# Optimization experiments

Measured on AMD Instinct MI355X. Metric: run time of the kernel, lower is better.

The kernel has to match this reference:

```python
import jax, jax.numpy as jnp
import numpy as np

B, S, D_IN, D_OUT = 4, 2048, 2048, 2048
E, R, TOP_K = 8, 8, 2
ALPHA = 16.0
SCALE = ALPHA / R  # alpha / r


def setup_inputs() -> dict:
    key = jax.random.key(0)
    ks = jax.random.split(key, 6)
    x = jax.random.normal(ks[0], (B, S, D_IN), dtype=jnp.float32)
    # base frozen linear: torch Linear weight [out, in], bias [out]
    W_base = jax.random.normal(ks[1], (D_OUT, D_IN), dtype=jnp.float32) / np.sqrt(D_IN)
    b_base = jax.random.normal(ks[2], (D_OUT,), dtype=jnp.float32) * 0.01
    # router: Linear(in_features, num_experts, bias=False) -> weight [E, in]
    W_router = jax.random.normal(ks[3], (E, D_IN), dtype=jnp.float32) / np.sqrt(D_IN)
    # LoRA experts: A [E, r, in], B [E, out, r] (torch inits B to zero; use small
    # random values so outputs/grads are non-trivial -- math is identical)
    A_w = jax.random.normal(ks[4], (E, R, D_IN), dtype=jnp.float32) / np.sqrt(D_IN)
    B_w = jax.random.normal(ks[5], (E, D_OUT, R), dtype=jnp.float32) * 0.02
    return {"x": x, "W_base": W_base, "b_base": b_base,
            "W_router": W_router, "A_w": A_w, "B_w": B_w}


def reference(x, W_base, b_base, W_router, A_w, B_w):
    # frozen base linear: [B,S,out]
    y = jnp.einsum('bsd,od->bso', x, W_base) + b_base
    # router: logits [B,S,E] -> top-k + softmax over the k selected logits
    logits = jnp.einsum('bsd,ed->bse', x, W_router)
    topk_vals, topk_idx = jax.lax.top_k(logits, TOP_K)       # [B,S,k]
    gates = jax.nn.softmax(topk_vals, axis=-1)               # [B,S,k]
    # all-experts LoRA compute (matches the original dense-stack semantics)
    h = jnp.einsum('bsd,erd->bser', x, A_w)                  # [B,S,E,r]
    expert_outs = jnp.einsum('bser,eor->bseo', h, B_w) * SCALE  # [B,S,E,out]
    # gather the top-k expert outputs and combine with gates
    topk_outs = jnp.take_along_axis(expert_outs, topk_idx[..., None], axis=2)  # [B,S,k,out]
    fused = jnp.sum(topk_outs * gates[..., None], axis=2)    # [B,S,out]
    return y + fused
```

## Files before the change

### kernel.cpp

```cpp
#include <hip/hip_runtime.h>

typedef unsigned short u16;
typedef __attribute__((ext_vector_type(8))) short short8;
typedef __attribute__((ext_vector_type(4))) float f32x4;

#define GLL16(g, l) __builtin_amdgcn_global_load_lds(                         \
    (const __attribute__((address_space(1))) void*)(g),                        \
    (__attribute__((address_space(3))) void*)(l), 16, 0, 0)

__device__ __forceinline__ u16 f2bf(float f) {
  union { float f; unsigned u; } v; v.f = f;
  unsigned u = v.u;
  return (u16)((u + 0x7FFFu + ((u >> 16) & 1u)) >> 16);
}

__device__ __forceinline__ float bf2f(u16 u) {
  union { unsigned u; float f; } v; v.u = ((unsigned)u) << 16;
  return v.f;
}

__device__ __forceinline__ ushort4 cvt4(float4 v) {
  ushort4 o; o.x = f2bf(v.x); o.y = f2bf(v.y); o.z = f2bf(v.z); o.w = f2bf(v.w);
  return o;
}

__global__ __launch_bounds__(512) void k_pre(
    const float* __restrict__ x, const float* __restrict__ Wr,
    const float* __restrict__ Wb, const float* __restrict__ Aw,
    const float* __restrict__ Bw,
    u16* __restrict__ xbf, float* __restrict__ logits,
    u16* __restrict__ wbf, u16* __restrict__ aabf, u16* __restrict__ bmt)
{
  __shared__ float wlds[16384];
  {
    const float4* src = (const float4*)Wr;
    float4* dst = (float4*)wlds;
    int t = threadIdx.x;
#pragma unroll
    for (int i = 0; i < 8; ++i) dst[t + i * 512] = src[t + i * 512];
  }
  __syncthreads();
  const int wave = threadIdx.x >> 6, lane = threadIdx.x & 63;
  const float4* wv = (const float4*)wlds;
#pragma unroll 1
  for (int s = 0; s < 2; ++s) {
    int tok = blockIdx.x * 16 + wave * 2 + s;
    const float4* xrow = (const float4*)(x + tok * 2048);
    ushort4* orow = (ushort4*)(xbf + tok * 2048);
    float acc[8];
#pragma unroll
    for (int e = 0; e < 8; ++e) acc[e] = 0.f;
#pragma unroll 1
    for (int i = 0; i < 8; ++i) {
      float4 xv = xrow[lane + i * 64];
      orow[lane + i * 64] = cvt4(xv);
#pragma unroll
      for (int e = 0; e < 8; ++e) {
        float4 b = wv[e * 512 + lane + i * 64];
        acc[e] += xv.x * b.x + xv.y * b.y + xv.z * b.z + xv.w * b.w;
      }
    }
#pragma unroll
    for (int e = 0; e < 8; ++e) {
      float v = acc[e];
#pragma unroll
      for (int off = 32; off > 0; off >>= 1) v += __shfl_xor(v, off, 64);
      acc[e] = v;
    }
    if (lane == 0) {
#pragma unroll
      for (int e = 0; e < 8; ++e) logits[tok * 8 + e] = acc[e];
    }
  }
  const int tidg = blockIdx.x * 512 + threadIdx.x;
  {
    const float4* src = (const float4*)Wb;
    ushort4* dst = (ushort4*)wbf;
#pragma unroll
    for (int i = 0; i < 4; ++i)
      dst[tidg + i * 262144] = cvt4(src[tidg + i * 262144]);
  }
  if (tidg < 32768) {
    ((ushort4*)aabf)[tidg] = cvt4(((const float4*)Aw)[tidg]);
  }
  if (tidg < 2048) {
    const int n = tidg;
#pragma unroll
    for (int e = 0; e < 8; ++e) {
      const float4* src = (const float4*)(Bw + e * 16384 + n * 8);
      ushort4* dst = (ushort4*)(bmt + n * 64 + e * 8);
      dst[0] = cvt4(src[0]);
      dst[1] = cvt4(src[1]);
    }
  }
}

__global__ __launch_bounds__(256) void k_hgemm(
    const u16* __restrict__ xbf, const u16* __restrict__ aabf,
    u16* __restrict__ P)
{
  __shared__ u16 As[256 * 64];
  __shared__ u16 Bs[64 * 64];
  int t = threadIdx.x, wave = t >> 6, lane = t & 63;
  int mBase = blockIdx.x * 256;
  int ks = blockIdx.y;
  int fr = lane & 15, fg = lane >> 4;
  int lrow = lane >> 3, lcol = (lane & 7) * 8;
  f32x4 zero = {0.f, 0.f, 0.f, 0.f};
  f32x4 acc[4][4];
#pragma unroll
  for (int i = 0; i < 4; ++i)
#pragma unroll
    for (int j = 0; j < 4; ++j) acc[i][j] = zero;
#pragma unroll 1
  for (int it = 0; it < 4; ++it) {
    int k0 = ks * 256 + it * 64;
    __syncthreads();
#pragma unroll
    for (int cc = 0; cc < 8; ++cc) {
      int c = wave * 8 + cc;
      GLL16(xbf + (mBase + c * 8 + lrow) * 2048 + k0 + lcol, &As[c * 512]);
    }
#pragma unroll
    for (int cc = 0; cc < 2; ++cc) {
      int c = wave * 2 + cc;
      GLL16(aabf + (c * 8 + lrow) * 2048 + k0 + lcol, &Bs[c * 512]);
    }
    __syncthreads();
#pragma unroll
    for (int kk = 0; kk < 2; ++kk) {
      short8 a[4], bfr[4];
#pragma unroll
      for (int i = 0; i < 4; ++i)
        a[i] = *(const short8*)&As[(wave * 64 + i * 16 + fr) * 64 + kk * 32 + fg * 8];
#pragma unroll
      for (int j = 0; j < 4; ++j)
        bfr[j] = *(const short8*)&Bs[(j * 16 + fr) * 64 + kk * 32 + fg * 8];
#pragma unroll
      for (int i = 0; i < 4; ++i)
#pragma unroll
        for (int j = 0; j < 4; ++j)
          acc[i][j] = __builtin_amdgcn_mfma_f32_16x16x32_bf16(a[i], bfr[j], acc[i][j], 0, 0, 0);
    }
  }
#pragma unroll
  for (int i = 0; i < 4; ++i)
#pragma unroll
    for (int j = 0; j < 4; ++j)
#pragma unroll
      for (int r = 0; r < 4; ++r) {
        int m = mBase + wave * 64 + i * 16 + fg * 4 + r;
        int n = j * 16 + fr;
        P[(ks * 8192 + m) * 64 + n] = f2bf(acc[i][j][r]);
      }
}

__global__ __launch_bounds__(256) void k_topk(
    const float* __restrict__ logits, const u16* __restrict__ P,
    u16* __restrict__ G)
{
  int t = threadIdx.x, wave = t >> 6, lane = t & 63;
  int tok = blockIdx.x * 4 + wave;
  const float* lg = logits + tok * 8;
  float la[8];
#pragma unroll
  for (int e = 0; e < 8; ++e) la[e] = lg[e];
  float v0 = la[0]; int i0 = 0;
#pragma unroll
  for (int e = 1; e < 8; ++e) { if (la[e] > v0) { v0 = la[e]; i0 = e; } }
  float v1 = -3.4e38f; int i1 = 0;
#pragma unroll
  for (int e = 0; e < 8; ++e) { if (e != i0 && la[e] > v1) { v1 = la[e]; i1 = e; } }
  float ex = expf(v1 - v0);
  float inv = 1.f / (1.f + ex);
  float gate0 = inv, gate1 = ex * inv;
  int e = lane >> 3;
  float h = 0.f;
#pragma unroll
  for (int ks = 0; ks < 8; ++ks) h += bf2f(P[(ks * 8192 + tok) * 64 + lane]);
  float g = (e == i0) ? gate0 : ((e == i1) ? gate1 : 0.f);
  G[tok * 64 + lane] = f2bf(2.0f * g * h);
}

__global__ __launch_bounds__(256, 2) void k_main(
    const u16* __restrict__ xbf, const u16* __restrict__ wbf,
    const u16* __restrict__ G, const u16* __restrict__ BmT,
    const float* __restrict__ bias, float* __restrict__ out)
{
  __shared__ u16 lds[40960];
  const int tid = threadIdx.x;
  const int w = tid >> 6, lane = tid & 63;
  const int fr = lane & 15, fg = lane >> 4;
  const int wr = w >> 1, wc = w & 1;

  const int b0 = blockIdx.x;
  const int xcd = b0 & 7, i = b0 >> 3;
  const int mBase = (xcd * 8 + (i >> 3)) * 128;
  const int nBase = (i & 7) * 256;

  const int rl = lane >> 3;
  const int ce = ((lane & 7) ^ rl) << 3;
  const int swz = (fr & 7) << 3;
  const int colk0 = (fg * 8) ^ swz;
  const int colk1 = (32 + fg * 8) ^ swz;
  const int aOff = (wr * 64 + fr) * 64;
  const int bOff = (wc * 128 + fr) * 64;

  const u16* pA = xbf + (mBase + w * 8 + rl) * 2048 + ce;
  const u16* pB = wbf + (nBase + w * 8 + rl) * 2048 + ce;

  f32x4 acc[4][8];
  const f32x4 zero = {0.f, 0.f, 0.f, 0.f};
#pragma unroll
  for (int mi = 0; mi < 4; ++mi)
#pragma unroll
    for (int nj = 0; nj < 8; ++nj) acc[mi][nj] = zero;

  short8 a[4][2];
  short8 U[2][2], V[2][2];

#define LGKM(N) asm volatile("s_waitcnt lgkmcnt(" #N ")" ::: "memory")
#define VMC(N)  asm volatile("s_waitcnt vmcnt(" #N ")" ::: "memory")
#define BAR()   __builtin_amdgcn_s_barrier()

#define SA() { GLL16(pA,          lds + w * 512);                             \
               GLL16(pA + 65536,  lds + 2048 + w * 512);                      \
               GLL16(pA + 131072, lds + 4096 + w * 512);                      \
               GLL16(pA + 196608, lds + 6144 + w * 512);                      \
               pA += 64; }
#define SB_LO(BOFF) { GLL16(pB,          lds + (BOFF) + w * 512);             \
                      GLL16(pB + 65536,  lds + (BOFF) + 2048 + w * 512);      \
                      GLL16(pB + 131072, lds + (BOFF) + 4096 + w * 512);      \
                      GLL16(pB + 196608, lds + (BOFF) + 6144 + w * 512); }
#define SB_HI(BOFF) { GLL16(pB + 262144, lds + (BOFF) + 8192 + w * 512);      \
                      GLL16(pB + 327680, lds + (BOFF) + 10240 + w * 512);     \
                      GLL16(pB + 393216, lds + (BOFF) + 12288 + w * 512);     \
                      GLL16(pB + 458752, lds + (BOFF) + 14336 + w * 512);     \
                      pB += 64; }

#define RDA()                                                                 \
  _Pragma("unroll")                                                           \
  for (int mi = 0; mi < 4; ++mi) {                                            \
    a[mi][0] = *(const short8*)(lds + aOff + mi * 1024 + colk0);              \
    a[mi][1] = *(const short8*)(lds + aOff + mi * 1024 + colk1);              \
  }

#define RDB2(DST, BOFF, NJ0)                                                  \
  DST[0][0] = *(const short8*)(lds + (BOFF) + bOff + (NJ0) * 1024 + colk0);   \
  DST[0][1] = *(const short8*)(lds + (BOFF) + bOff + (NJ0) * 1024 + colk1);   \
  DST[1][0] = *(const short8*)(lds + (BOFF) + bOff + ((NJ0)+1) * 1024 + colk0);\
  DST[1][1] = *(const short8*)(lds + (BOFF) + bOff + ((NJ0)+1) * 1024 + colk1);

#define MFMAP(BV, NJ0)                                                        \
  __builtin_amdgcn_s_setprio(1);                                              \
  _Pragma("unroll")                                                           \
  for (int kk = 0; kk < 2; ++kk)                                              \
    _Pragma("unroll")                                                         \
    for (int mi = 0; mi < 4; ++mi)                                            \
      _Pragma("unroll")                                                       \
      for (int j = 0; j < 2; ++j)                                             \
        acc[mi][(NJ0) + j] = __builtin_amdgcn_mfma_f32_16x16x32_bf16(         \
            a[mi][kk], BV[j][kk], acc[mi][(NJ0) + j], 0, 0, 0);               \
  __builtin_amdgcn_s_setprio(0);

#define TILE(BCUR, BNXT, SA_STMT, SBL_STMT, SBH_STMT)                         \
  {                                                                           \
                                                                      \
    VMC(0);                                                                   \
    BAR();                                                                    \
    RDB2(U, BCUR, 0)                                                          \
    RDA()                                                                     \
    RDB2(V, BCUR, 2)                                                          \
    LGKM(4);                                                                  \
    MFMAP(U, 0)                                                               \
    BAR();                                                                    \
                                                                      \
    SA_STMT                                                                   \
    RDB2(U, BCUR, 4)                                                          \
    LGKM(4);                                                                  \
    MFMAP(V, 2)                                                               \
                                                                      \
    SBL_STMT                                                                  \
    RDB2(V, BCUR, 6)                                                          \
    LGKM(4);                                                                  \
    MFMAP(U, 4)                                                               \
                                                                      \
    SBH_STMT                                                                  \
    LGKM(0);                                                                  \
    MFMAP(V, 6)                                                               \
  }

  SA()
  SB_LO(8192) SB_HI(8192)

#pragma unroll 1
  for (int tt = 0; tt < 15; ++tt) {
    TILE(8192, 24576, SA(), SB_LO(24576), SB_HI(24576))
    TILE(24576, 8192, SA(), SB_LO(8192), SB_HI(8192))
  }
  TILE(8192, 24576, SA(), SB_LO(24576), SB_HI(24576))
  {
    const u16* pG = G + (mBase + w * 8 + rl) * 64 + ce;
    const u16* pT = BmT + (nBase + w * 8 + rl) * 64 + ce;
    TILE(24576, 8192,
         { GLL16(pG,        lds + w * 512);
           GLL16(pG + 2048, lds + 2048 + w * 512);
           GLL16(pG + 4096, lds + 4096 + w * 512);
           GLL16(pG + 6144, lds + 6144 + w * 512); },
         { GLL16(pT,        lds + 8192 + w * 512);
           GLL16(pT + 2048, lds + 8192 + 2048 + w * 512);
           GLL16(pT + 4096, lds + 8192 + 4096 + w * 512);
           GLL16(pT + 6144, lds + 8192 + 6144 + w * 512); },
         { GLL16(pT + 8192,  lds + 8192 + 8192 + w * 512);
           GLL16(pT + 10240, lds + 8192 + 10240 + w * 512);
           GLL16(pT + 12288, lds + 8192 + 12288 + w * 512);
           GLL16(pT + 14336, lds + 8192 + 14336 + w * 512); })
  }
  TILE(8192, 24576, {}, {}, {})

#pragma unroll
  for (int nj = 0; nj < 8; ++nj) {
    const int n = nBase + wc * 128 + nj * 16 + fr;
    const float bv = bias[n];
#pragma unroll
    for (int mi = 0; mi < 4; ++mi) {
      const int m = mBase + wr * 64 + mi * 16 + fg * 4;
#pragma unroll
      for (int r = 0; r < 4; ++r)
        out[(m + r) * 2048 + n] = acc[mi][nj][r] + bv;
    }
  }
#undef TILE
#undef MFMAP
#undef RDB2
#undef RDA
#undef SB_HI
#undef SB_LO
#undef SA
#undef BAR
#undef VMC
#undef LGKM
}

extern "C" void kernel_launch(void* const* d_in, const int* in_sizes, int n_in,
                              void* d_out, int out_size, void* d_ws, size_t ws_size,
                              hipStream_t stream) {
  const float* x  = (const float*)d_in[0];
  const float* Wb = (const float*)d_in[1];
  const float* bb = (const float*)d_in[2];
  const float* Wr = (const float*)d_in[3];
  const float* Aw = (const float*)d_in[4];
  const float* Bw = (const float*)d_in[5];

  char* ws = (char*)d_ws;
  u16*   xbf  = (u16*)  (ws + 0);
  u16*   wbf  = (u16*)  (ws + 33554432);
  u16*   aabf = (u16*)  (ws + 41943040);
  u16*   bmt  = (u16*)  (ws + 42205184);
  float* lgt  = (float*)(ws + 42467328);
  u16*   G    = (u16*)  (ws + 42729472);
  u16*   P   = (u16*)d_out;
  float* out = (float*)d_out;

  hipLaunchKernelGGL(k_pre,   dim3(512),   dim3(512), 0, stream,
                     x, Wr, Wb, Aw, Bw, xbf, lgt, wbf, aabf, bmt);
  hipLaunchKernelGGL(k_hgemm, dim3(32, 8), dim3(256), 0, stream, xbf, aabf, P);
  hipLaunchKernelGGL(k_topk,  dim3(2048),  dim3(256), 0, stream, lgt, P, G);
  hipLaunchKernelGGL(k_main,  dim3(512),   dim3(256), 0, stream,
                     xbf, wbf, G, bmt, bb, out);
}
```

Measured before the change: 108.9 us.

## Shrink main GEMM tile to 128x128 and raise occupancy to three blocks

```diff
diff --git a/kernel.cpp b/kernel.cpp
--- a/kernel.cpp
+++ b/kernel.cpp
@@ -182,21 +182,21 @@
   G[tok * 64 + lane] = f2bf(2.0f * g * h);
 }
 
-__global__ __launch_bounds__(256, 2) void k_main(
+__global__ __launch_bounds__(256, 3) void k_main(
     const u16* __restrict__ xbf, const u16* __restrict__ wbf,
     const u16* __restrict__ G, const u16* __restrict__ BmT,
     const float* __restrict__ bias, float* __restrict__ out)
 {
-  __shared__ u16 lds[40960];
+  __shared__ u16 lds[24576];
   const int tid = threadIdx.x;
   const int w = tid >> 6, lane = tid & 63;
   const int fr = lane & 15, fg = lane >> 4;
   const int wr = w >> 1, wc = w & 1;
 
   const int b0 = blockIdx.x;
-  const int xcd = b0 & 7, i = b0 >> 3;
-  const int mBase = (xcd * 8 + (i >> 3)) * 128;
-  const int nBase = (i & 7) * 256;
+  const int xcd = b0 & 7, ii = b0 >> 3;
+  const int mBase = (xcd * 8 + (ii >> 4)) * 128;
+  const int nBase = (ii & 15) * 128;
 
   const int rl = lane >> 3;
   const int ce = ((lane & 7) ^ rl) << 3;
@@ -204,17 +204,17 @@
   const int colk0 = (fg * 8) ^ swz;
   const int colk1 = (32 + fg * 8) ^ swz;
   const int aOff = (wr * 64 + fr) * 64;
-  const int bOff = (wc * 128 + fr) * 64;
-
-  const u16* pA = xbf + (mBase + w * 8 + rl) * 2048 + ce;
-  const u16* pB = wbf + (nBase + w * 8 + rl) * 2048 + ce;
-
-  f32x4 acc[4][8];
+  const int bOff = (wc * 64 + fr) * 64;
+
+  const u16* pA = xbf + (mBase + w * 32 + rl) * 2048 + ce;
+  const u16* pB = wbf + (nBase + w * 32 + rl) * 2048 + ce;
+
+  f32x4 acc[4][4];
   const f32x4 zero = {0.f, 0.f, 0.f, 0.f};
 #pragma unroll
   for (int mi = 0; mi < 4; ++mi)
 #pragma unroll
-    for (int nj = 0; nj < 8; ++nj) acc[mi][nj] = zero;
+    for (int nj = 0; nj < 4; ++nj) acc[mi][nj] = zero;
 
   short8 a[4][2];
   short8 U[2][2], V[2][2];
@@ -223,20 +223,16 @@
 #define VMC(N)  asm volatile("s_waitcnt vmcnt(" #N ")" ::: "memory")
 #define BAR()   __builtin_amdgcn_s_barrier()
 
-#define SA() { GLL16(pA,          lds + w * 512);                             \
-               GLL16(pA + 65536,  lds + 2048 + w * 512);                      \
-               GLL16(pA + 131072, lds + 4096 + w * 512);                      \
-               GLL16(pA + 196608, lds + 6144 + w * 512);                      \
+#define SA() { GLL16(pA,         lds + w * 2048);                             \
+               GLL16(pA + 16384, lds + w * 2048 + 512);                       \
+               GLL16(pA + 32768, lds + w * 2048 + 1024);                      \
+               GLL16(pA + 49152, lds + w * 2048 + 1536);                      \
                pA += 64; }
-#define SB_LO(BOFF) { GLL16(pB,          lds + (BOFF) + w * 512);             \
-                      GLL16(pB + 65536,  lds + (BOFF) + 2048 + w * 512);      \
-                      GLL16(pB + 131072, lds + (BOFF) + 4096 + w * 512);      \
-                      GLL16(pB + 196608, lds + (BOFF) + 6144 + w * 512); }
-#define SB_HI(BOFF) { GLL16(pB + 262144, lds + (BOFF) + 8192 + w * 512);      \
-                      GLL16(pB + 327680, lds + (BOFF) + 10240 + w * 512);     \
-                      GLL16(pB + 393216, lds + (BOFF) + 12288 + w * 512);     \
-                      GLL16(pB + 458752, lds + (BOFF) + 14336 + w * 512);     \
-                      pB += 64; }
+#define SB(BOFF) { GLL16(pB,         lds + (BOFF) + w * 2048);                \
+                   GLL16(pB + 16384, lds + (BOFF) + w * 2048 + 512);          \
+                   GLL16(pB + 32768, lds + (BOFF) + w * 2048 + 1024);         \
+                   GLL16(pB + 49152, lds + (BOFF) + w * 2048 + 1536);         \
+                   pB += 64; }
 
 #define RDA()                                                                 \
   _Pragma("unroll")                                                           \
@@ -263,7 +259,7 @@
             a[mi][kk], BV[j][kk], acc[mi][(NJ0) + j], 0, 0, 0);               \
   __builtin_amdgcn_s_setprio(0);
 
-#define TILE(BCUR, BNXT, SA_STMT, SBL_STMT, SBH_STMT)                         \
+#define TILE(BCUR, SBS, SAS)                                                  \
   {                                                                           \
                                                                       \
     VMC(0);                                                                   \
@@ -275,52 +271,39 @@
     MFMAP(U, 0)                                                               \
     BAR();                                                                    \
                                                                       \
-    SA_STMT                                                                   \
-    RDB2(U, BCUR, 4)                                                          \
-    LGKM(4);                                                                  \
+    SAS                                                                       \
+    SBS                                                                       \
+    LGKM(0);                                                                  \
     MFMAP(V, 2)                                                               \
-                                                                      \
-    SBL_STMT                                                                  \
-    RDB2(V, BCUR, 6)                                                          \
-    LGKM(4);                                                                  \
-    MFMAP(U, 4)                                                               \
-                                                                      \
-    SBH_STMT                                                                  \
-    LGKM(0);                                                                  \
-    MFMAP(V, 6)                                                               \
   }
 
   SA()
-  SB_LO(8192) SB_HI(8192)
+  SB(8192)
 
 #pragma unroll 1
   for (int tt = 0; tt < 15; ++tt) {
-    TILE(8192, 24576, SA(), SB_LO(24576), SB_HI(24576))
-    TILE(24576, 8192, SA(), SB_LO(8192), SB_HI(8192))
-  }
-  TILE(8192, 24576, SA(), SB_LO(24576), SB_HI(24576))
+    TILE(8192, SB(16384), SA())
+    TILE(16384, SB(8192), SA())
+  }
+  TILE(8192, SB(16384), SA())
   {
-    const u16* pG = G + (mBase + w * 8 + rl) * 64 + ce;
-    const u16* pT = BmT + (nBase + w * 8 + rl) * 64 + ce;
-    TILE(24576, 8192,
-         { GLL16(pG,        lds + w * 512);
-           GLL16(pG + 2048, lds + 2048 + w * 512);
-           GLL16(pG + 4096, lds + 4096 + w * 512);
-           GLL16(pG + 6144, lds + 6144 + w * 512); },
-         { GLL16(pT,        lds + 8192 + w * 512);
-           GLL16(pT + 2048, lds + 8192 + 2048 + w * 512);
-           GLL16(pT + 4096, lds + 8192 + 4096 + w * 512);
-           GLL16(pT + 6144, lds + 8192 + 6144 + w * 512); },
-         { GLL16(pT + 8192,  lds + 8192 + 8192 + w * 512);
-           GLL16(pT + 10240, lds + 8192 + 10240 + w * 512);
-           GLL16(pT + 12288, lds + 8192 + 12288 + w * 512);
-           GLL16(pT + 14336, lds + 8192 + 14336 + w * 512); })
-  }
-  TILE(8192, 24576, {}, {}, {})
-
-#pragma unroll
-  for (int nj = 0; nj < 8; ++nj) {
-    const int n = nBase + wc * 128 + nj * 16 + fr;
+    const u16* pG = G + (mBase + w * 32 + rl) * 64 + ce;
+    const u16* pT = BmT + (nBase + w * 32 + rl) * 64 + ce;
+    TILE(16384,
+         { GLL16(pT,        lds + 8192 + w * 2048);
+           GLL16(pT + 512,  lds + 8192 + w * 2048 + 512);
+           GLL16(pT + 1024, lds + 8192 + w * 2048 + 1024);
+           GLL16(pT + 1536, lds + 8192 + w * 2048 + 1536); },
+         { GLL16(pG,        lds + w * 2048);
+           GLL16(pG + 512,  lds + w * 2048 + 512);
+           GLL16(pG + 1024, lds + w * 2048 + 1024);
+           GLL16(pG + 1536, lds + w * 2048 + 1536); })
+  }
+  TILE(8192, {}, {})
+
+#pragma unroll
+  for (int nj = 0; nj < 4; ++nj) {
+    const int n = nBase + wc * 64 + nj * 16 + fr;
     const float bv = bias[n];
 #pragma unroll
     for (int mi = 0; mi < 4; ++mi) {
@@ -334,8 +317,7 @@
 #undef MFMAP
 #undef RDB2
 #undef RDA
-#undef SB_HI
-#undef SB_LO
+#undef SB
 #undef SA
 #undef BAR
 #undef VMC
@@ -366,6 +348,6 @@
                      x, Wr, Wb, Aw, Bw, xbf, lgt, wbf, aabf, bmt);
   hipLaunchKernelGGL(k_hgemm, dim3(32, 8), dim3(256), 0, stream, xbf, aabf, P);
   hipLaunchKernelGGL(k_topk,  dim3(2048),  dim3(256), 0, stream, lgt, P, G);
-  hipLaunchKernelGGL(k_main,  dim3(512),   dim3(256), 0, stream,
+  hipLaunchKernelGGL(k_main,  dim3(1024),  dim3(256), 0, stream,
                      xbf, wbf, G, bmt, bb, out);
 }
```

Result: slower. 121.1 us (+11.2%).
